# Kernel tuning notes

Hardware: AMD Instinct MI355X
Metric: run time of the kernel (lower is better)

The kernel has to match this reference:

```python
import jax, jax.numpy as jnp
import numpy as np

VOCAB, EMB_DIM = 50000, 300
HIDDEN, OUT_DIM, N_ASPECTS = 256, 3, 8
BATCH, SEQ = 8192, 128


def setup_inputs() -> dict:
    key = jax.random.key(0)
    k1, k2, k3, k4, k5, k6, k7 = jax.random.split(key, 7)
    input_ids = jax.random.randint(k1, (BATCH, SEQ), 0, VOCAB, dtype=jnp.int64 if jax.config.jax_enable_x64 else jnp.int32)
    aspect_id = jax.random.randint(k2, (BATCH,), 0, N_ASPECTS, dtype=jnp.int32)
    emb = jax.random.normal(k3, (VOCAB, EMB_DIM), dtype=jnp.float32)
    # Per-aspect 2-layer MLP params, stacked along aspect axis. PyTorch Linear
    # init scale ~ U(-1/sqrt(fan_in), 1/sqrt(fan_in)).
    s1 = 1.0 / np.sqrt(EMB_DIM)
    s2 = 1.0 / np.sqrt(HIDDEN)
    W1 = jax.random.uniform(k4, (N_ASPECTS, EMB_DIM, HIDDEN), jnp.float32, -s1, s1)
    b1 = jax.random.uniform(k5, (N_ASPECTS, HIDDEN), jnp.float32, -s1, s1)
    W2 = jax.random.uniform(k6, (N_ASPECTS, HIDDEN, OUT_DIM), jnp.float32, -s2, s2)
    b2 = jax.random.uniform(k7, (N_ASPECTS, OUT_DIM), jnp.float32, -s2, s2)
    return {"input_ids": input_ids, "aspect_id": aspect_id, "emb": emb,
            "W1": W1, "b1": b1, "W2": W2, "b2": b2}


def reference(input_ids, aspect_id, emb, W1, b1, W2, b2):
    # Embedding lookup + mean-pool over sequence -> [B, EMB_DIM]
    x = emb[input_ids].mean(axis=1)
    # Run every sample through every aspect MLP (A is tiny: 8), then select.
    # Same math as per-sample routed MLP, but as A batched GEMMs.
    h = jax.nn.relu(jnp.einsum('bd,adh->abh', x, W1) + b1[:, None, :])  # [A,B,H]
    o = jnp.einsum('abh,aho->abo', h, W2) + b2[:, None, :]              # [A,B,O]
    # Select per-sample expert output: [B, OUT_DIM]
    o_b = jnp.transpose(o, (1, 0, 2))  # [B, A, O]
    return jnp.take_along_axis(o_b, aspect_id[:, None, None], axis=1)[:, 0, :]
```

## Files before the change

### kernel.cpp

```cpp
#include <hip/hip_runtime.h>

constexpr int EMB_DIM   = 300;
constexpr int HIDDEN    = 256;
constexpr int OUT_DIM   = 3;
constexpr int SEQ       = 128;
constexpr int N_ASPECTS = 8;
constexpr int TILE      = 32;
constexpr int MTILE     = 16;

__device__ __forceinline__ unsigned int bfbits(float f) {
  unsigned int u = __float_as_uint(f);
  return (u + 0x7fffu + ((u >> 16) & 1u)) >> 16;
}
__device__ __forceinline__ unsigned int pack2(float lo, float hi) {
  return bfbits(lo) | (bfbits(hi) << 16);
}
__device__ __forceinline__ float blo(unsigned int u) { return __uint_as_float(u << 16); }
__device__ __forceinline__ float bhi(unsigned int u) { return __uint_as_float(u & 0xffff0000u); }

__global__ __launch_bounds__(1024) void prep_kernel(
    const float* __restrict__ emb, unsigned short* __restrict__ embA,
    unsigned short* __restrict__ embB, int vocab,
    const int* __restrict__ aspect, int B, int* __restrict__ perm, int nperm) {
  const int t = threadIdx.x;
  const int lane = t & 63, wave = t >> 6;

  if (blockIdx.x != 0) {
    const int cw = (blockIdx.x - 1) * 16 + wave;
    const int nw = (gridDim.x - 1) * 16;
    for (int v = cw; v < vocab; v += nw) {
      const float4* __restrict__ src = (const float4*)(emb + (size_t)v * EMB_DIM);
      float4 p = src[lane];
      uint2 w;
      w.x = pack2(p.x, p.y); w.y = pack2(p.z, p.w);
      ((uint2*)(embA + (size_t)v * 256))[lane] = w;
      if (lane < 11) {
        float4 q = src[64 + lane];
        uint2 u;
        u.x = pack2(q.x, q.y); u.y = pack2(q.z, q.w);
        ((uint2*)(embB + (size_t)v * 64))[lane] = u;
      }
    }
    return;
  }

  __shared__ int wcnt[16][N_ASPECTS];
  __shared__ int cur[16][N_ASPECTS];

  for (int i = t; i < nperm; i += 1024) perm[i] = -1;

  int my_a[8];
  int cnt[N_ASPECTS];
#pragma unroll
  for (int q = 0; q < N_ASPECTS; ++q) cnt[q] = 0;
#pragma unroll
  for (int k = 0; k < 8; ++k) {
    int s = t + k * 1024;
    int a = (s < B) ? aspect[s] : -1;
    my_a[k] = a;
#pragma unroll
    for (int q = 0; q < N_ASPECTS; ++q) cnt[q] += (a == q);
  }
#pragma unroll
  for (int q = 0; q < N_ASPECTS; ++q) {
    int c = cnt[q];
    for (int off = 32; off > 0; off >>= 1) c += __shfl_down(c, off);
    if (lane == 0) wcnt[wave][q] = c;
  }
  __syncthreads();
  if (t == 0) {
    int base = 0;
    for (int q = 0; q < N_ASPECTS; ++q) {
      int tot = 0;
      for (int w = 0; w < 16; ++w) { cur[w][q] = base + tot; tot += wcnt[w][q]; }
      base += ((tot + TILE - 1) / TILE) * TILE;
    }
  }
  __syncthreads();

#pragma unroll
  for (int k = 0; k < 8; ++k) {
    int a = my_a[k];
    int s = t + k * 1024;
#pragma unroll
    for (int q = 0; q < N_ASPECTS; ++q) {
      unsigned long long m = __ballot(a == q);
      if (a == q) {
        int rank = __popcll(m & ((1ull << lane) - 1ull));
        int pos = cur[wave][q] + rank;
        perm[pos] = s;
        if (rank == __popcll(m) - 1) cur[wave][q] = pos + 1;
      }
    }
  }
}

__global__ __launch_bounds__(256) void pool_kernel(
    const int* __restrict__ ids, const unsigned short* __restrict__ embA,
    const unsigned short* __restrict__ embB, float* __restrict__ x, int B) {
  const int wave = threadIdx.x >> 6, lane = threadIdx.x & 63;
  const int b = blockIdx.x * 4 + wave;
  if (b >= B) return;

  int r0 = ids[(size_t)b * SEQ + lane];
  int r1 = ids[(size_t)b * SEQ + lane + 64];

#pragma unroll
  for (int k = 2; k <= 128; k <<= 1) {
#pragma unroll
    for (int j = k >> 1; j >= 1; j >>= 1) {
      if (j == 64) {
        int lo = min(r0, r1), hi = max(r0, r1);
        r0 = lo; r1 = hi;
      } else {
        const bool up0 = ((lane & k) == 0);
        const bool up1 = (((lane + 64) & k) == 0);
        const bool side = ((lane & j) == 0);
        int o0 = __shfl_xor(r0, j);
        int o1 = __shfl_xor(r1, j);
        r0 = (side == up0) ? min(r0, o0) : max(r0, o0);
        r1 = (side == up1) ? min(r1, o1) : max(r1, o1);
      }
    }
  }

  __shared__ int sA[4][SEQ];
  __shared__ int sB[4][SEQ];
  sA[wave][lane]      = r0 << 9;
  sA[wave][lane + 64] = r1 << 9;
  sB[wave][lane]      = r0 << 7;
  sB[wave][lane + 64] = r1 << 7;
  __syncthreads();

  float a0 = 0.f, a1 = 0.f, a2 = 0.f, a3 = 0.f;
  const char* __restrict__ baseA = (const char*)embA + (size_t)lane * 8;
#pragma unroll 8
  for (int s = 0; s < SEQ; ++s) {
    uint2 v = *(const uint2*)(baseA + sA[wave][s]);
    a0 += blo(v.x); a1 += bhi(v.x); a2 += blo(v.y); a3 += bhi(v.y);
  }

  const int myTok = lane / 11;
  const int mySub = lane - myTok * 11;
  float c0 = 0.f, c1 = 0.f, c2 = 0.f, c3 = 0.f;
  if (lane < 44) {
    const char* __restrict__ baseB = (const char*)embB + (size_t)mySub * 8;
#pragma unroll 8
    for (int s = 0; s < SEQ; s += 4) {
      uint2 v = *(const uint2*)(baseB + sB[wave][s + myTok]);
      c0 += blo(v.x); c1 += bhi(v.x); c2 += blo(v.y); c3 += bhi(v.y);
    }
  }
  c0 += __shfl_down(c0, 22); c1 += __shfl_down(c1, 22);
  c2 += __shfl_down(c2, 22); c3 += __shfl_down(c3, 22);
  c0 += __shfl_down(c0, 11); c1 += __shfl_down(c1, 11);
  c2 += __shfl_down(c2, 11); c3 += __shfl_down(c3, 11);

  const float sc = 1.0f / (float)SEQ;
  float4* __restrict__ xr = (float4*)(x + (size_t)b * EMB_DIM);
  xr[lane] = make_float4(a0 * sc, a1 * sc, a2 * sc, a3 * sc);
  if (lane < 11) {
    float4* __restrict__ xb = (float4*)(x + (size_t)b * EMB_DIM + 256);
    xb[lane] = make_float4(c0 * sc, c1 * sc, c2 * sc, c3 * sc);
  }
}

__global__ __launch_bounds__(256) void mlp_kernel(
    const float* __restrict__ x, const int* __restrict__ aspect,
    const int* __restrict__ perm,
    const float* __restrict__ W1, const float* __restrict__ b1,
    const float* __restrict__ W2, const float* __restrict__ b2,
    float* __restrict__ out) {
  const int t = threadIdx.x;
  const int wave = t >> 6, lane = t & 63;
  const int g = wave >> 1;
  const int kw = wave & 1;
  const int start = blockIdx.x * MTILE;

  __shared__ int ss[MTILE];
  __shared__ float xch[2][8][64][4];

  if (t < MTILE) ss[t] = perm[start + t];
  __syncthreads();
  const int s0 = ss[0];
  if (s0 < 0) return;
  const int a = aspect[s0];

  int smp[8];
  const float* xrow[8];
#pragma unroll
  for (int s = 0; s < 8; ++s) {
    int m = __builtin_amdgcn_readfirstlane(ss[g * 8 + s]);
    smp[s] = m;
    xrow[s] = x + (size_t)(m < 0 ? s0 : m) * EMB_DIM;
  }

  const float4* __restrict__ w1r =
      (const float4*)(W1 + (size_t)a * EMB_DIM * HIDDEN) + lane;
  float4 acc[8];
  if (kw == 0) {
    const float4 bb = ((const float4*)(b1 + a * HIDDEN))[lane];
#pragma unroll
    for (int s = 0; s < 8; ++s) acc[s] = bb;
  } else {
#pragma unroll
    for (int s = 0; s < 8; ++s) acc[s] = make_float4(0.f, 0.f, 0.f, 0.f);
  }
  const int d0 = kw ? 160 : 0;
  const int d1 = kw ? EMB_DIM : 160;
  for (int d = d0; d < d1; d += 4) {
    float4 xv[8];
#pragma unroll
    for (int s = 0; s < 8; ++s) xv[s] = *(const float4*)(xrow[s] + d);
#pragma unroll
    for (int dd = 0; dd < 4; ++dd) {
      const float4 w = w1r[(size_t)(d + dd) * (HIDDEN / 4)];
#pragma unroll
      for (int s = 0; s < 8; ++s) {
        const float xs = dd == 0 ? xv[s].x : dd == 1 ? xv[s].y
                        : dd == 2 ? xv[s].z : xv[s].w;
        acc[s].x = fmaf(xs, w.x, acc[s].x);
        acc[s].y = fmaf(xs, w.y, acc[s].y);
        acc[s].z = fmaf(xs, w.z, acc[s].z);
        acc[s].w = fmaf(xs, w.w, acc[s].w);
      }
    }
  }

  if (kw == 0) {
#pragma unroll
    for (int i = 0; i < 4; ++i)
      *(float4*)&xch[g][4 + i][lane][0] = acc[4 + i];
  } else {
#pragma unroll
    for (int i = 0; i < 4; ++i)
      *(float4*)&xch[g][i][lane][0] = acc[i];
  }
  __syncthreads();

  const float4* __restrict__ w2p =
      (const float4*)(W2 + (size_t)a * HIDDEN * OUT_DIM + lane * 12);
  const float4 w2a = w2p[0];
  const float4 w2b = w2p[1];
  const float4 w2c = w2p[2];

  float4 own[4];
  int ms[4];
  if (kw == 0) {
    own[0] = acc[0]; own[1] = acc[1]; own[2] = acc[2]; own[3] = acc[3];
    ms[0] = smp[0]; ms[1] = smp[1]; ms[2] = smp[2]; ms[3] = smp[3];
  } else {
    own[0] = acc[4]; own[1] = acc[5]; own[2] = acc[6]; own[3] = acc[7];
    ms[0] = smp[4]; ms[1] = smp[5]; ms[2] = smp[6]; ms[3] = smp[7];
  }
  const int mys = 4 * kw;

  float p[4][OUT_DIM];
#pragma unroll
  for (int i = 0; i < 4; ++i) {
    const float4 pr = *(const float4*)&xch[g][mys + i][lane][0];
    const float h0 = fmaxf(own[i].x + pr.x, 0.f);
    const float h1 = fmaxf(own[i].y + pr.y, 0.f);
    const float h2 = fmaxf(own[i].z + pr.z, 0.f);
    const float h3 = fmaxf(own[i].w + pr.w, 0.f);
    p[i][0] = fmaf(h0, w2a.x, fmaf(h1, w2a.w, fmaf(h2, w2b.z, h3 * w2c.y)));
    p[i][1] = fmaf(h0, w2a.y, fmaf(h1, w2b.x, fmaf(h2, w2b.w, h3 * w2c.z)));
    p[i][2] = fmaf(h0, w2a.z, fmaf(h1, w2b.y, fmaf(h2, w2c.x, h3 * w2c.w)));
  }
#pragma unroll
  for (int off = 32; off > 0; off >>= 1)
#pragma unroll
    for (int i = 0; i < 4; ++i) {
      p[i][0] += __shfl_down(p[i][0], off);
      p[i][1] += __shfl_down(p[i][1], off);
      p[i][2] += __shfl_down(p[i][2], off);
    }

  if (lane == 0) {
    const float g0 = b2[a * OUT_DIM + 0];
    const float g1 = b2[a * OUT_DIM + 1];
    const float g2 = b2[a * OUT_DIM + 2];
#pragma unroll
    for (int i = 0; i < 4; ++i) {
      if (ms[i] >= 0) {
        float* o = out + (size_t)ms[i] * OUT_DIM;
        o[0] = p[i][0] + g0;
        o[1] = p[i][1] + g1;
        o[2] = p[i][2] + g2;
      }
    }
  }
}

extern "C" void kernel_launch(void* const* d_in, const int* in_sizes, int n_in,
                              void* d_out, int out_size, void* d_ws, size_t ws_size,
                              hipStream_t stream) {
  const int*   ids    = (const int*)d_in[0];
  const int*   aspect = (const int*)d_in[1];
  const float* emb    = (const float*)d_in[2];
  const float* W1     = (const float*)d_in[3];
  const float* b1     = (const float*)d_in[4];
  const float* W2     = (const float*)d_in[5];
  const float* b2     = (const float*)d_in[6];
  float*       out    = (float*)d_out;

  const int B     = in_sizes[1];
  const int nemb  = in_sizes[2];
  const int VOCAB = nemb / EMB_DIM;
  const int nblk  = (B + TILE - 1) / TILE + N_ASPECTS;
  const int nperm = nblk * TILE;

  float* x    = (float*)d_ws;
  int*   perm = (int*)((char*)d_ws + (size_t)B * EMB_DIM * sizeof(float));
  size_t offA = ((size_t)B * EMB_DIM * sizeof(float) + (size_t)nperm * 4 + 511) & ~(size_t)511;
  unsigned short* embA = (unsigned short*)((char*)d_ws + offA);
  unsigned short* embB = embA + (size_t)VOCAB * 256;

  prep_kernel<<<513, 1024, 0, stream>>>(emb, embA, embB, VOCAB,
                                        aspect, B, perm, nperm);
  pool_kernel<<<(B + 3) / 4, 256, 0, stream>>>(ids, embA, embB, x, B);
  mlp_kernel<<<nperm / MTILE, 256, 0, stream>>>(x, aspect, perm, W1, b1, W2, b2, out);
}
```

Measured before the change: 135.9 us.

## Widen gather loads to 16B, prefetch next group, merge tail loop into main

Reworks the embedding mean-pool gather so each lane loads 16-byte bf16 chunks for two tokens per iteration, with half-waves splitting tokens and a shuffle reduction combining them. The tail-column loop is folded into the same software-pipelined loop that prefetches the next group's loads while accumulating the current ones. The __syncthreads is also removed, since each wave only reads its own shared index row. The aim is fewer, wider memory instructions and more loads in flight, at the cost of extra registers and a cross-lane reduction. Lanes 44-63 now issue redundant tail loads, which only makes extra loads and does not change results.

```diff
diff --git a/kernel.cpp b/kernel.cpp
--- a/kernel.cpp
+++ b/kernel.cpp
@@ -130,35 +130,54 @@
   sA[wave][lane + 64] = r1 << 9;
   sB[wave][lane]      = r0 << 7;
   sB[wave][lane + 64] = r1 << 7;
-  __syncthreads();
+
+  const int half = lane >> 5;
+  const int l32  = lane & 31;
+  int myTok = lane / 11, mySub = lane - myTok * 11;
+  if (myTok > 3) { myTok = 3; mySub = 10; }
+  const char* __restrict__ pA = (const char*)embA + (size_t)l32 * 16;
+  const char* __restrict__ pB = (const char*)embB + (size_t)mySub * 8;
 
   float a0 = 0.f, a1 = 0.f, a2 = 0.f, a3 = 0.f;
-  const char* __restrict__ baseA = (const char*)embA + (size_t)lane * 8;
-#pragma unroll 8
-  for (int s = 0; s < SEQ; ++s) {
-    uint2 v = *(const uint2*)(baseA + sA[wave][s]);
-    a0 += blo(v.x); a1 += bhi(v.x); a2 += blo(v.y); a3 += bhi(v.y);
-  }
-
-  const int myTok = lane / 11;
-  const int mySub = lane - myTok * 11;
+  float a4 = 0.f, a5 = 0.f, a6 = 0.f, a7 = 0.f;
   float c0 = 0.f, c1 = 0.f, c2 = 0.f, c3 = 0.f;
-  if (lane < 44) {
-    const char* __restrict__ baseB = (const char*)embB + (size_t)mySub * 8;
-#pragma unroll 8
-    for (int s = 0; s < SEQ; s += 4) {
-      uint2 v = *(const uint2*)(baseB + sB[wave][s + myTok]);
-      c0 += blo(v.x); c1 += bhi(v.x); c2 += blo(v.y); c3 += bhi(v.y);
-    }
-  }
+
+  uint4 vA0 = *(const uint4*)(pA + sA[wave][half]);
+  uint4 vA1 = *(const uint4*)(pA + sA[wave][2 + half]);
+  uint2 vB  = *(const uint2*)(pB + sB[wave][myTok]);
+
+#pragma unroll 2
+  for (int g = 0; g < 32; ++g) {
+    uint4 nA0, nA1; uint2 nB;
+    if (g < 31) {
+      const int base = 4 * (g + 1);
+      nA0 = *(const uint4*)(pA + sA[wave][base + half]);
+      nA1 = *(const uint4*)(pA + sA[wave][base + 2 + half]);
+      nB  = *(const uint2*)(pB + sB[wave][base + myTok]);
+    }
+    a0 += blo(vA0.x); a1 += bhi(vA0.x); a2 += blo(vA0.y); a3 += bhi(vA0.y);
+    a4 += blo(vA0.z); a5 += bhi(vA0.z); a6 += blo(vA0.w); a7 += bhi(vA0.w);
+    a0 += blo(vA1.x); a1 += bhi(vA1.x); a2 += blo(vA1.y); a3 += bhi(vA1.y);
+    a4 += blo(vA1.z); a5 += bhi(vA1.z); a6 += blo(vA1.w); a7 += bhi(vA1.w);
+    c0 += blo(vB.x);  c1 += bhi(vB.x);  c2 += blo(vB.y);  c3 += bhi(vB.y);
+    vA0 = nA0; vA1 = nA1; vB = nB;
+  }
+
+  a0 += __shfl_down(a0, 32); a1 += __shfl_down(a1, 32);
+  a2 += __shfl_down(a2, 32); a3 += __shfl_down(a3, 32);
+  a4 += __shfl_down(a4, 32); a5 += __shfl_down(a5, 32);
+  a6 += __shfl_down(a6, 32); a7 += __shfl_down(a7, 32);
   c0 += __shfl_down(c0, 22); c1 += __shfl_down(c1, 22);
   c2 += __shfl_down(c2, 22); c3 += __shfl_down(c3, 22);
   c0 += __shfl_down(c0, 11); c1 += __shfl_down(c1, 11);
   c2 += __shfl_down(c2, 11); c3 += __shfl_down(c3, 11);
 
   const float sc = 1.0f / (float)SEQ;
-  float4* __restrict__ xr = (float4*)(x + (size_t)b * EMB_DIM);
-  xr[lane] = make_float4(a0 * sc, a1 * sc, a2 * sc, a3 * sc);
+  if (lane < 32) {
+    float4* __restrict__ xr = (float4*)(x + (size_t)b * EMB_DIM);
+    xr[lane * 2]     = make_float4(a0 * sc, a1 * sc, a2 * sc, a3 * sc);
+    xr[lane * 2 + 1] = make_float4(a4 * sc, a5 * sc, a6 * sc, a7 * sc);
+  }
   if (lane < 11) {
     float4* __restrict__ xb = (float4*)(x + (size_t)b * EMB_DIM + 256);
     xb[lane] = make_float4(c0 * sc, c1 * sc, c2 * sc, c3 * sc);
```

Result: slower. 142.5 us (+4.9%).
